# Kernel optimization log

Measured on AMD Instinct MI355X. Metric: run time of the kernel, lower is better.

## Reference

```python
import jax, jax.numpy as jnp
import numpy as np

SCALES = (32.0, 64.0, 128.0, 256.0)
RATIOS = (0.5, 1.0, 2.0)
STRIDE = 16
KEEP = 2000          # pre-NMS top-k
TOPK = 300           # post-NMS top-k
MIN_SIZE = 16.0
SCORE_THRESH = 0.05
NMS_THRESH = 0.7


def static_anchors():
    a = []
    for s in SCALES:
        for r in RATIOS:
            w = s * r ** 0.5
            h = s / r ** 0.5
            a.append((-w / 2, -h / 2, w / 2, h / 2))
    return jnp.asarray(a, jnp.float32)  # [12,4]


def generate_anchors(h, w):
    base = static_anchors()
    sx = jnp.arange(w, dtype=jnp.float32) * STRIDE + STRIDE / 2
    sy = jnp.arange(h, dtype=jnp.float32) * STRIDE + STRIDE / 2
    yy, xx = jnp.meshgrid(sy, sx, indexing='ij')
    xs, ys = xx.reshape(-1), yy.reshape(-1)
    shifts = jnp.stack((xs, ys, xs, ys), axis=1)            # [HW,4]
    return (base[None, :, :] + shifts[:, None, :]).reshape(-1, 4)  # [HW*12,4]


def apply_deltas(anchors, d):
    # bbox reg weights are all 1.0
    aw = anchors[..., 2] - anchors[..., 0]
    ah = anchors[..., 3] - anchors[..., 1]
    ax = anchors[..., 0] + aw * 0.5
    ay = anchors[..., 1] + ah * 0.5
    x = ax + d[..., 0] * aw
    y = ay + d[..., 1] * ah
    w = aw * jnp.exp(d[..., 2])
    h = ah * jnp.exp(d[..., 3])
    return jnp.stack((x - w * 0.5, y - h * 0.5, x + w * 0.5, y + h * 0.5), axis=-1)


def conv2d(x, w, b, pad):
    y = jax.lax.conv_general_dilated(x, w, (1, 1), [(pad, pad), (pad, pad)],
                                     dimension_numbers=('NCHW', 'OIHW', 'NCHW'))
    return y + b[None, :, None, None]


def nms_fixed(boxes, scores, valid):
    # boxes already sorted by descending score; greedy NMS with fixed shapes.
    area = (boxes[:, 2] - boxes[:, 0]) * (boxes[:, 3] - boxes[:, 1])
    lt = jnp.maximum(boxes[:, None, :2], boxes[None, :, :2])
    rb = jnp.minimum(boxes[:, None, 2:], boxes[None, :, 2:])
    wh = jnp.clip(rb - lt, 0.0)
    inter = wh[..., 0] * wh[..., 1]
    iou = inter / jnp.maximum(area[:, None] + area[None, :] - inter, 1e-6)
    n = boxes.shape[0]

    def body(i, state):
        keep, supp = state
        k = jnp.logical_and(~supp[i], True)
        keep = keep.at[i].set(k)
        supp = jnp.logical_or(supp, jnp.logical_and(k, iou[i] > NMS_THRESH))
        return keep, supp

    keep, _ = jax.lax.fori_loop(0, n, body, (jnp.zeros(n, bool), ~valid))
    masked = jnp.where(keep, scores, -jnp.inf)
    top_s, top_i = jax.lax.top_k(masked, TOPK)
    ok = top_s > -jnp.inf
    out_boxes = jnp.where(ok[:, None], boxes[top_i], 0.0)
    out_scores = jnp.where(ok, top_s, 0.0)
    return out_boxes, out_scores


def rpn_forward(fx, w1, b1, w2, b2, w3, b3, img_h, img_w):
    _, _, H, W = fx.shape
    x = jax.nn.relu(conv2d(fx, w1, b1, 1))        # [1,512,H,W]
    ox = conv2d(x, w2, b2, 0)                     # [1,12,H,W]
    ax = conv2d(x, w3, b3, 0)                     # [1,48,H,W]
    anchors = generate_anchors(H, W)              # [A,4]
    ox = jnp.transpose(ox, (0, 2, 3, 1)).reshape(-1)                     # [A]
    ax = jnp.transpose(ax.reshape(1, 12, 4, H, W), (0, 3, 4, 1, 2)).reshape(-1, 4)  # [A,4]
    px = apply_deltas(anchors, ax)                # [A,4]
    s = jax.nn.sigmoid(ox)
    top_s, idx = jax.lax.top_k(s, KEEP)           # pre-NMS filter
    b = px[idx]
    x1 = jnp.clip(b[:, 0], 0.0, img_w)
    x2 = jnp.clip(b[:, 2], 0.0, img_w)
    y1 = jnp.clip(b[:, 1], 0.0, img_h)
    y2 = jnp.clip(b[:, 3], 0.0, img_h)
    boxes = jnp.stack((x1, y1, x2, y2), axis=1)
    valid = ((x2 - x1) >= MIN_SIZE) & ((y2 - y1) >= MIN_SIZE) & (top_s >= SCORE_THRESH)
    out_boxes, out_scores = nms_fixed(boxes, top_s, valid)
    return jnp.concatenate((out_boxes, out_scores[:, None]), axis=1)  # [TOPK,5]


def setup_inputs() -> dict:
    key = jax.random.key(0)
    ks = jax.random.split(key, 4)
    fx = jax.random.normal(ks[0], (1, 1024, 64, 64), jnp.float32)
    w1 = jax.random.normal(ks[1], (512, 1024, 3, 3), jnp.float32) * 0.01
    w2 = jax.random.normal(ks[2], (12, 512, 1, 1), jnp.float32) * 0.01
    w3 = jax.random.normal(ks[3], (48, 512, 1, 1), jnp.float32) * 0.01
    return {"fx": fx, "w1": w1, "b1": jnp.zeros((512,), jnp.float32),
            "w2": w2, "b2": jnp.zeros((12,), jnp.float32),
            "w3": w3, "b3": jnp.zeros((48,), jnp.float32),
            "img_h": 1024, "img_w": 1024}


def reference(fx, w1, b1, w2, b2, w3, b3, img_h, img_w):
    return rpn_forward(fx, w1, b1, w2, b2, w3, b3, float(img_h), float(img_w))
```

## Files before the change

kernel.cpp:

```cpp
#include <hip/hip_runtime.h>
#include <math.h>

typedef unsigned int u32;
typedef unsigned long long u64;
typedef unsigned short u16;

typedef float f32x16 __attribute__((ext_vector_type(16)));
typedef short bf16x8 __attribute__((ext_vector_type(8)));

#define A_TOTAL 49152
#define NKEEP 2000
#define NTOPK 300
#define SORTN 4096

#define OFF_PACC   0u
#define OFF_POX    8388608u
#define OFF_BOXES  16777216u
#define OFF_SCORES 17563648u
#define OFF_HIST   17760256u
#define OFF_KEYS   18022400u
#define OFF_CAND5  18055168u
#define OFF_MASK   18096128u
#define OFF_MISC   18620416u

__global__ __launch_bounds__(256) void k_init(u32* __restrict__ hist, u64* __restrict__ keys,
                                              u32* __restrict__ misc, float* __restrict__ out) {
    int t = blockIdx.x * 256 + threadIdx.x;
    if (t < 65536) hist[t] = 0u;
    if (t < SORTN) keys[t] = 0ull;
    if (t < NTOPK * 5) out[t] = 0.f;
    if (t == 0) misc[0] = 0u;
}

__device__ __forceinline__ u16 f2bf(float v) {
    u32 u = __float_as_uint(v);
    return (u16)((u + 0x7FFFu + ((u >> 16) & 1u)) >> 16);
}
__device__ __forceinline__ float bf2f(u16 h) { return __uint_as_float(((u32)h) << 16); }
__device__ __forceinline__ void split3(float v, u16& h, u16& m, u16& l) {
    h = f2bf(v);
    float r1 = v - bf2f(h);
    m = f2bf(r1);
    float r2 = r1 - bf2f(m);
    l = f2bf(r2);
}
__device__ __forceinline__ bf16x8 ldsfrag(const u16* p) {
    const u64* q = (const u64*)p;
    union { u64 w[2]; bf16x8 v; } x;
    x.w[0] = q[0];
    x.w[1] = q[1];
    return x.v;
}

__global__ __launch_bounds__(512, 4) void k_conv1m(const float* __restrict__ fx, const float* __restrict__ w1,
                                                   float* __restrict__ pacc) {
    __shared__ u16 sA[3 * 9472];
    __shared__ u16 sB[3 * 3600];
    const int tid = threadIdx.x;
    const int lane = tid & 63;
    const int wid = tid >> 6;
    const int cgw = wid >> 2;
    const int pgw = wid & 3;
    const int n = lane & 31;
    const int g = lane >> 5;
    const int bpx = blockIdx.x;
    const int y0 = (bpx >> 2) * 8, x0 = (bpx & 3) * 16;
    const int co0 = blockIdx.y * 64;
    const int kh = blockIdx.z;
    const int ci_base = kh * 512;

    int wg[9], wlA[9];
    u32 wbm = 0u;
#pragma unroll
    for (int j = 0; j < 9; j++) {
        int e = tid + j * 512;
        int co = e / 72, q = e - co * 72;
        int f0 = q * 2;
        int t0 = f0 % 9, c0 = f0 / 9;
        wg[j] = co * 9216 + f0;
        wlA[j] = co * 148 + t0 * 16 + c0;
        if (t0 == 8) wbm |= (1u << j);
    }
    int fg0[6], fl[6];
#pragma unroll
    for (int j = 0; j < 6; j++) {
        int idx = tid + j * 512;
        bool wr = idx < 2880;
        int ci = idx / 180, rem = idx - ci * 180;
        int hy = rem / 18, hx = rem - hy * 18;
        int gy = y0 + hy - 1, gx = x0 + hx - 1;
        bool ok = wr && gy >= 0 && gy < 64 && gx >= 0 && gx < 64;
        fg0[j] = ok ? (ci * 4096 + gy * 64 + gx) : -1;
        fl[j] = wr ? (rem * 20 + ci) : -1;
    }

    f32x16 acc;
    double accD[16];
#pragma unroll
    for (int i = 0; i < 16; i++) { acc[i] = 0.f; accD[i] = 0.0; }

    float pw[18], pf[6];
    {
        const float* wp = w1 + (size_t)co0 * 9216 + (size_t)ci_base * 9;
#pragma unroll
        for (int j = 0; j < 9; j++) { pw[2 * j] = wp[wg[j]]; pw[2 * j + 1] = wp[wg[j] + 1]; }
        const float* fp = fx + (size_t)ci_base * 4096;
#pragma unroll
        for (int j = 0; j < 6; j++) pf[j] = (fg0[j] >= 0) ? fp[fg0[j]] : 0.f;
    }

#pragma unroll 1
    for (int c = 0; c < 32; c++) {
        __syncthreads();
#pragma unroll
        for (int j = 0; j < 9; j++) {
            u16 h, m, l;
            int iA = wlA[j];
            int iB = iA + (((wbm >> j) & 1u) ? -127 : 16);
            split3(pw[2 * j], h, m, l);
            sA[iA] = h; sA[9472 + iA] = m; sA[18944 + iA] = l;
            split3(pw[2 * j + 1], h, m, l);
            sA[iB] = h; sA[9472 + iB] = m; sA[18944 + iB] = l;
        }
#pragma unroll
        for (int j = 0; j < 6; j++) {
            if (fl[j] >= 0) {
                u16 h, m, l;
                split3(pf[j], h, m, l);
                sB[fl[j]] = h; sB[3600 + fl[j]] = m; sB[7200 + fl[j]] = l;
            }
        }
        __syncthreads();
        if (c < 31) {
            const float* wp = w1 + (size_t)co0 * 9216 + (size_t)(ci_base + (c + 1) * 16) * 9;
#pragma unroll
            for (int j = 0; j < 9; j++) { pw[2 * j] = wp[wg[j]]; pw[2 * j + 1] = wp[wg[j] + 1]; }
            const float* fp = fx + (size_t)(ci_base + (c + 1) * 16) * 4096;
#pragma unroll
            for (int j = 0; j < 6; j++) pf[j] = (fg0[j] >= 0) ? fp[fg0[j]] : 0.f;
        }

#pragma unroll 1
        for (int dy = 0; dy < 3; dy++) {
#pragma unroll
            for (int dx = 0; dx < 3; dx++) {
                const int tap = dy * 3 + dx;
                const int aoff = (cgw * 32 + n) * 148 + tap * 16 + g * 8;
                bf16x8 ah = ldsfrag(&sA[aoff]);
                bf16x8 am = ldsfrag(&sA[9472 + aoff]);
                bf16x8 al = ldsfrag(&sA[18944 + aoff]);
                const int loc = (pgw * 2 + (n >> 4) + dy) * 18 + (n & 15) + dx;
                const int boff = loc * 20 + g * 8;
                bf16x8 bh = ldsfrag(&sB[boff]);
                bf16x8 bm = ldsfrag(&sB[3600 + boff]);
                bf16x8 bl = ldsfrag(&sB[7200 + boff]);
                acc = __builtin_amdgcn_mfma_f32_32x32x16_bf16(ah, bh, acc, 0, 0, 0);
                acc = __builtin_amdgcn_mfma_f32_32x32x16_bf16(ah, bm, acc, 0, 0, 0);
                acc = __builtin_amdgcn_mfma_f32_32x32x16_bf16(am, bh, acc, 0, 0, 0);
                acc = __builtin_amdgcn_mfma_f32_32x32x16_bf16(ah, bl, acc, 0, 0, 0);
                acc = __builtin_amdgcn_mfma_f32_32x32x16_bf16(am, bm, acc, 0, 0, 0);
                acc = __builtin_amdgcn_mfma_f32_32x32x16_bf16(al, bh, acc, 0, 0, 0);
            }
#pragma unroll
            for (int i = 0; i < 16; i++) { accD[i] += (double)acc[i]; acc[i] = 0.f; }
        }
    }

    {
        int p = pgw * 32 + n;
        int py = p >> 4, pxx = p & 15;
        int gp = (y0 + py) * 64 + x0 + pxx;
        const int row_hi = 4 * g;
#pragma unroll
        for (int rg = 0; rg < 16; rg++) {
            int co = co0 + cgw * 32 + (rg & 3) + 8 * (rg >> 2) + row_hi;
            pacc[(size_t)kh * 2097152 + (size_t)co * 4096 + gp] = (float)accD[rg];
        }
    }
}

__global__ __launch_bounds__(256) void k_comb(float* __restrict__ x, const float* __restrict__ p1,
                                              const float* __restrict__ b1) {
    int i = blockIdx.x * 256 + threadIdx.x;
    double v = (double)x[i] + (double)p1[i] + (double)b1[i >> 12];
    x[i] = fmaxf((float)v, 0.f);
}

__global__ __launch_bounds__(256) void k_conv23(const float* __restrict__ x,
                                                const float* __restrict__ w2, const float* __restrict__ w3,
                                                double* __restrict__ pox) {
    __shared__ float xs[32 * 64];
    __shared__ float wsh[60 * 128];
    const int tid = threadIdx.x;
    const int px0 = blockIdx.x * 64;
    const int cib = blockIdx.y * 128;
    const int px = tid & 63;
    const int og = tid >> 6;

#pragma unroll
    for (int k = 0; k < 30; k++) {
        int e = tid + k * 256;
        int o = e >> 7, ci = e & 127;
        float wv = (o < 12) ? w2[o * 512 + cib + ci] : w3[(size_t)(o - 12) * 512 + cib + ci];
        wsh[o * 128 + ci] = wv;
    }

    double acc[15];
#pragma unroll
    for (int j = 0; j < 15; j++) acc[j] = 0.0;

#pragma unroll 1
    for (int ch = 0; ch < 4; ch++) {
        __syncthreads();
#pragma unroll
        for (int k = 0; k < 8; k++) {
            int e = tid + k * 256;
            int ci = e >> 6, p = e & 63;
            xs[ci * 64 + p] = x[(size_t)(cib + ch * 32 + ci) * 4096 + px0 + p];
        }
        __syncthreads();
#pragma unroll 1
        for (int ci = 0; ci < 32; ci++) {
            double xd = (double)xs[ci * 64 + px];
            const float* wrow = &wsh[ch * 32 + ci];
#pragma unroll
            for (int j = 0; j < 15; j++)
                acc[j] = fma(xd, (double)wrow[(og * 15 + j) * 128], acc[j]);
        }
    }
#pragma unroll
    for (int j = 0; j < 15; j++) {
        int o = og * 15 + j;
        pox[((size_t)o * 4 + blockIdx.y) * 4096 + px0 + px] = acc[j];
    }
}

__global__ __launch_bounds__(256) void k_boxes(const double* __restrict__ pox,
                                               const float* __restrict__ b2, const float* __restrict__ b3,
                                               const int* __restrict__ imh, const int* __restrict__ imw,
                                               float* __restrict__ boxes, float* __restrict__ scores,
                                               u32* __restrict__ hist) {
    int idx = blockIdx.x * 256 + threadIdx.x;
    if (idx >= A_TOTAL) return;
    int px = idx / 12, a = idx - px * 12;

    double t = 0.0;
#pragma unroll
    for (int q = 0; q < 4; q++) t += pox[((size_t)a * 4 + q) * 4096 + px];
    float o = (float)(t + (double)b2[a]);
    float s = (float)(1.0 / (1.0 + exp(-(double)o)));
    scores[idx] = s;
    atomicAdd(&hist[__float_as_uint(s) >> 16], 1u);

    float d[4];
#pragma unroll
    for (int c = 0; c < 4; c++) {
        int oo = 12 + a * 4 + c;
        double u = 0.0;
#pragma unroll
        for (int q = 0; q < 4; q++) u += pox[((size_t)oo * 4 + q) * 4096 + px];
        d[c] = (float)(u + (double)b3[a * 4 + c]);
    }

    int py = px >> 6, pxx = px & 63;
    double cx = pxx * 16.0 + 8.0, cy = py * 16.0 + 8.0;
    int si = a / 3, ri = a - si * 3;
    double scale = (double)(32 << si);
    double ratio = 0.5 * (double)(1 << ri);
    double sq = sqrt(ratio);
    double aw = scale * sq, ah = scale / sq;
    double xc = cx + (double)d[0] * aw;
    double yc = cy + (double)d[1] * ah;
    double wv = aw * exp((double)d[2]);
    double hv = ah * exp((double)d[3]);
    float W = (float)imw[0], H = (float)imh[0];
    float x1 = fminf(fmaxf((float)(xc - wv * 0.5), 0.f), W);
    float x2 = fminf(fmaxf((float)(xc + wv * 0.5), 0.f), W);
    float y1 = fminf(fmaxf((float)(yc - hv * 0.5), 0.f), H);
    float y2 = fminf(fmaxf((float)(yc + hv * 0.5), 0.f), H);
    boxes[(size_t)idx * 4 + 0] = x1;
    boxes[(size_t)idx * 4 + 1] = y1;
    boxes[(size_t)idx * 4 + 2] = x2;
    boxes[(size_t)idx * 4 + 3] = y2;
}

__global__ __launch_bounds__(256) void k_scanhist(const u32* __restrict__ hist, u32* __restrict__ misc) {
    __shared__ u32 csum[256];
    __shared__ u32 cb[256];
    __shared__ int s_cidx;
    __shared__ u32 s_cacc;
    int t = threadIdx.x;
    u32 sum = 0;
    const uint4* h4 = (const uint4*)(hist + t * 256);
    for (int j = 0; j < 64; j++) { uint4 v = h4[j]; sum += v.x + v.y + v.z + v.w; }
    csum[t] = sum;
    __syncthreads();
    if (t == 0) {
        u32 acc = 0;
        int c = 255;
        for (; c > 0; c--) {
            if (acc + csum[c] >= NKEEP) break;
            acc += csum[c];
        }
        s_cidx = c;
        s_cacc = acc;
    }
    __syncthreads();
    cb[t] = hist[s_cidx * 256 + t];
    __syncthreads();
    if (t == 0) {
        u32 acc = s_cacc;
        int b = 255;
        for (; b > 0; b--) {
            acc += cb[b];
            if (acc >= NKEEP) break;
        }
        misc[1] = (u32)(s_cidx * 256 + b);
    }
}

__global__ __launch_bounds__(256) void k_compact(const float* __restrict__ scores, u32* __restrict__ misc,
                                                 u64* __restrict__ keys) {
    int idx = blockIdx.x * 256 + threadIdx.x;
    if (idx >= A_TOTAL) return;
    u32 bits = __float_as_uint(scores[idx]);
    if ((bits >> 16) >= misc[1]) {
        u32 slot = atomicAdd(&misc[0], 1u);
        if (slot < SORTN) keys[slot] = ((u64)bits << 32) | (u64)(~(u32)idx);
    }
}

__global__ __launch_bounds__(1024) void k_sort(const u64* __restrict__ keys, const float* __restrict__ boxes,
                                               float* __restrict__ cand5, u64* __restrict__ suppws) {
    __shared__ u64 lk[SORTN];
    int t = threadIdx.x;
#pragma unroll
    for (int r = 0; r < 4; r++) lk[r * 1024 + t] = keys[r * 1024 + t];
    for (int kk = 2; kk <= SORTN; kk <<= 1) {
        for (int jj = kk >> 1; jj > 0; jj >>= 1) {
            __syncthreads();
#pragma unroll
            for (int rep = 0; rep < 4; rep++) {
                int i = rep * 1024 + t;
                int ixj = i ^ jj;
                if (ixj > i) {
                    u64 a = lk[i], b = lk[ixj];
                    bool sw = ((i & kk) == 0) ? (a < b) : (a > b);
                    if (sw) { lk[i] = b; lk[ixj] = a; }
                }
            }
        }
    }
    __syncthreads();
#pragma unroll
    for (int rep = 0; rep < 2; rep++) {
        int i = rep * 1024 + t;
        bool suppb = true;
        float c0 = 0.f, c1 = 0.f, c2 = 0.f, c3 = 0.f, cs = 0.f;
        if (i < NKEEP) {
            u64 key = lk[i];
            u32 idx = ~(u32)(key & 0xFFFFFFFFull);
            cs = __uint_as_float((u32)(key >> 32));
            c0 = boxes[(size_t)idx * 4 + 0];
            c1 = boxes[(size_t)idx * 4 + 1];
            c2 = boxes[(size_t)idx * 4 + 2];
            c3 = boxes[(size_t)idx * 4 + 3];
            bool valid = ((c2 - c0) >= 16.f) && ((c3 - c1) >= 16.f) && (cs >= 0.05f);
            suppb = !valid;
        }
        cand5[i * 5 + 0] = c0;
        cand5[i * 5 + 1] = c1;
        cand5[i * 5 + 2] = c2;
        cand5[i * 5 + 3] = c3;
        cand5[i * 5 + 4] = cs;
        u64 bal = __ballot(suppb ? 1 : 0);
        if ((t & 63) == 0) suppws[i >> 6] = bal;
    }
}

__global__ __launch_bounds__(64) void k_mask(const float* __restrict__ cand5, u64* __restrict__ mask) {
    __shared__ float cb[64][5];
    int t = threadIdx.x;
    int bi = blockIdx.y, bj = blockIdx.x;
    int j = bj * 64 + t;
    {
        float b0 = cand5[j * 5 + 0], b1v = cand5[j * 5 + 1], b2v = cand5[j * 5 + 2], b3v = cand5[j * 5 + 3];
        cb[t][0] = b0; cb[t][1] = b1v; cb[t][2] = b2v; cb[t][3] = b3v;
        cb[t][4] = (b2v - b0) * (b3v - b1v);
    }
    __syncthreads();
    int i = bi * 64 + t;
    float r0 = cand5[i * 5 + 0], r1 = cand5[i * 5 + 1], r2 = cand5[i * 5 + 2], r3 = cand5[i * 5 + 3];
    float ra = (r2 - r0) * (r3 - r1);
    u64 bits = 0ull;
#pragma unroll 4
    for (int c = 0; c < 64; c++) {
        float lx = fmaxf(r0, cb[c][0]);
        float ly = fmaxf(r1, cb[c][1]);
        float rx = fminf(r2, cb[c][2]);
        float ry = fminf(r3, cb[c][3]);
        float w = fmaxf(rx - lx, 0.f);
        float h = fmaxf(ry - ly, 0.f);
        float inter = w * h;
        float iou = inter / fmaxf(ra + cb[c][4] - inter, 1e-6f);
        if (iou > 0.7f) bits |= (1ull << c);
    }
    mask[(size_t)i * 32 + bj] = bits;
}

__global__ __launch_bounds__(64) void k_scan(const u64* __restrict__ mask, const float* __restrict__ cand5,
                                             const u64* __restrict__ suppws, float* __restrict__ out) {
    int lane = threadIdx.x;
    u64 supp = (lane < 32) ? suppws[lane] : 0ull;
    u64 bufA[8], bufB[8];
    float dA[8], dB[8];
#pragma unroll
    for (int k = 0; k < 8; k++) {
        bufA[k] = (lane < 32) ? mask[(size_t)k * 32 + lane] : 0ull;
        dA[k] = (lane < 5) ? cand5[k * 5 + lane] : 0.f;
    }
    int kcount = 0;
    for (int gq = 0; gq < 256; gq++) {
        int base = gq * 8;
        if (gq < 255) {
            int nb = base + 8;
#pragma unroll
            for (int k = 0; k < 8; k++) {
                bufB[k] = (lane < 32) ? mask[(size_t)(nb + k) * 32 + lane] : 0ull;
                dB[k] = (lane < 5) ? cand5[(nb + k) * 5 + lane] : 0.f;
            }
        }
        int w = gq >> 3;
        u64 cur = __shfl(supp, w);
#pragma unroll
        for (int k = 0; k < 8; k++) {
            int i = base + k;
            if (i < NKEEP && !((cur >> (i & 63)) & 1ull)) {
                if (kcount < NTOPK) {
                    if (lane < 5) out[kcount * 5 + lane] = dA[k];
                    kcount++;
                }
                supp |= bufA[k];
                cur |= __shfl(bufA[k], w);
            }
        }
        if (kcount >= NTOPK) return;
#pragma unroll
        for (int k = 0; k < 8; k++) { bufA[k] = bufB[k]; dA[k] = dB[k]; }
    }
}

extern "C" void kernel_launch(void* const* d_in, const int* in_sizes, int n_in,
                              void* d_out, int out_size, void* d_ws, size_t ws_size,
                              hipStream_t stream) {
    (void)in_sizes; (void)n_in; (void)out_size; (void)ws_size;
    const float* fx = (const float*)d_in[0];
    const float* w1 = (const float*)d_in[1];
    const float* b1 = (const float*)d_in[2];
    const float* w2 = (const float*)d_in[3];
    const float* b2 = (const float*)d_in[4];
    const float* w3 = (const float*)d_in[5];
    const float* b3 = (const float*)d_in[6];
    const int* imh = (const int*)d_in[7];
    const int* imw = (const int*)d_in[8];

    char* ws = (char*)d_ws;
    float*  pacc   = (float*)(ws + OFF_PACC);
    double* pox    = (double*)(ws + OFF_POX);
    float*  boxes  = (float*)(ws + OFF_BOXES);
    float*  scores = (float*)(ws + OFF_SCORES);
    u32*    hist   = (u32*)(ws + OFF_HIST);
    u64*    keys   = (u64*)(ws + OFF_KEYS);
    float*  cand5  = (float*)(ws + OFF_CAND5);
    u64*    mask   = (u64*)(ws + OFF_MASK);
    u32*    misc   = (u32*)(ws + OFF_MISC);
    u64*    suppws = (u64*)(ws + OFF_MISC + 64);
    float*  out    = (float*)d_out;

    k_init<<<256, 256, 0, stream>>>(hist, keys, misc, out);
    k_conv1m<<<dim3(32, 8, 2), 512, 0, stream>>>(fx, w1, pacc);
    k_comb<<<8192, 256, 0, stream>>>(pacc, pacc + 2097152, b1);
    k_conv23<<<dim3(64, 4), 256, 0, stream>>>(pacc, w2, w3, pox);
    k_boxes<<<192, 256, 0, stream>>>(pox, b2, b3, imh, imw, boxes, scores, hist);
    k_scanhist<<<1, 256, 0, stream>>>(hist, misc);
    k_compact<<<192, 256, 0, stream>>>(scores, misc, keys);
    k_sort<<<1, 1024, 0, stream>>>(keys, boxes, cand5, suppws);
    k_mask<<<dim3(32, 32), 64, 0, stream>>>(cand5, mask);
    k_scan<<<1, 64, 0, stream>>>(mask, cand5, suppws, out);
}
```

Baseline: 560.8 us.

## Rework conv1 staging: paired weight stores, 2-deep fx prefetch, co-major block order

The 3-D grid becomes a 1-D grid ordered so that the eight output-channel blocks for the same pixel tile run next to each other, which is meant to improve L2 reuse of the feature map. Weight staging now pairs two consecutive input channels for the same tap and writes each of the three bf16 split planes with one 32-bit LDS store instead of two 16-bit stores. Feature loads are prefetched two chunks ahead to hide global latency. The launch bound no longer requests four blocks per CU, so the compiler may use more registers at the cost of occupancy, and the extra prefetch buffers add register pressure.

```diff
diff --git a/kernel.cpp b/kernel.cpp
--- a/kernel.cpp
+++ b/kernel.cpp
@@ -52,10 +52,11 @@
     return x.v;
 }
 
-__global__ __launch_bounds__(512, 4) void k_conv1m(const float* __restrict__ fx, const float* __restrict__ w1,
-                                                   float* __restrict__ pacc) {
+__global__ __launch_bounds__(512) void k_conv1m(const float* __restrict__ fx, const float* __restrict__ w1,
+                                                float* __restrict__ pacc) {
     __shared__ u16 sA[3 * 9472];
     __shared__ u16 sB[3 * 3600];
+    u32* const sA32 = (u32*)sA;
     const int tid = threadIdx.x;
     const int lane = tid & 63;
     const int wid = tid >> 6;
@@ -63,23 +64,23 @@
     const int pgw = wid & 3;
     const int n = lane & 31;
     const int g = lane >> 5;
-    const int bpx = blockIdx.x;
+    const int bid = blockIdx.x;
+    const int yb = bid & 7;
+    const int rest = bid >> 3;
+    const int bpx = rest & 31;
+    const int kh = rest >> 5;
     const int y0 = (bpx >> 2) * 8, x0 = (bpx & 3) * 16;
-    const int co0 = blockIdx.y * 64;
-    const int kh = blockIdx.z;
+    const int co0 = yb * 64;
     const int ci_base = kh * 512;
 
-    int wg[9], wlA[9];
-    u32 wbm = 0u;
+    int wgp[9], wlp[9];
 #pragma unroll
     for (int j = 0; j < 9; j++) {
-        int e = tid + j * 512;
-        int co = e / 72, q = e - co * 72;
-        int f0 = q * 2;
-        int t0 = f0 % 9, c0 = f0 / 9;
-        wg[j] = co * 9216 + f0;
-        wlA[j] = co * 148 + t0 * 16 + c0;
-        if (t0 == 8) wbm |= (1u << j);
+        int p = tid + j * 512;
+        int co = p / 72, q = p - co * 72;
+        int a = q & 7, b = q >> 3;
+        wgp[j] = co * 9216 + (2 * a) * 9 + b;
+        wlp[j] = co * 74 + b * 8 + a;
     }
     int fg0[6], fl[6];
 #pragma unroll
@@ -99,14 +100,18 @@
 #pragma unroll
     for (int i = 0; i < 16; i++) { acc[i] = 0.f; accD[i] = 0.0; }
 
-    float pw[18], pf[6];
+    float pw[18], pfA[6], pfB[6];
     {
         const float* wp = w1 + (size_t)co0 * 9216 + (size_t)ci_base * 9;
 #pragma unroll
-        for (int j = 0; j < 9; j++) { pw[2 * j] = wp[wg[j]]; pw[2 * j + 1] = wp[wg[j] + 1]; }
-        const float* fp = fx + (size_t)ci_base * 4096;
-#pragma unroll
-        for (int j = 0; j < 6; j++) pf[j] = (fg0[j] >= 0) ? fp[fg0[j]] : 0.f;
+        for (int j = 0; j < 9; j++) { pw[2 * j] = wp[wgp[j]]; pw[2 * j + 1] = wp[wgp[j] + 9]; }
+        const float* f0 = fx + (size_t)ci_base * 4096;
+        const float* f1 = fx + (size_t)(ci_base + 16) * 4096;
+#pragma unroll
+        for (int j = 0; j < 6; j++) {
+            pfA[j] = (fg0[j] >= 0) ? f0[fg0[j]] : 0.f;
+            pfB[j] = (fg0[j] >= 0) ? f1[fg0[j]] : 0.f;
+        }
     }
 
 #pragma unroll 1
@@ -114,19 +119,18 @@
         __syncthreads();
 #pragma unroll
         for (int j = 0; j < 9; j++) {
-            u16 h, m, l;
-            int iA = wlA[j];
-            int iB = iA + (((wbm >> j) & 1u) ? -127 : 16);
-            split3(pw[2 * j], h, m, l);
-            sA[iA] = h; sA[9472 + iA] = m; sA[18944 + iA] = l;
-            split3(pw[2 * j + 1], h, m, l);
-            sA[iB] = h; sA[9472 + iB] = m; sA[18944 + iB] = l;
+            u16 h0, m0, l0, h1, m1, l1;
+            split3(pw[2 * j], h0, m0, l0);
+            split3(pw[2 * j + 1], h1, m1, l1);
+            sA32[wlp[j]] = (u32)h0 | ((u32)h1 << 16);
+            sA32[4736 + wlp[j]] = (u32)m0 | ((u32)m1 << 16);
+            sA32[9472 + wlp[j]] = (u32)l0 | ((u32)l1 << 16);
         }
 #pragma unroll
         for (int j = 0; j < 6; j++) {
             if (fl[j] >= 0) {
                 u16 h, m, l;
-                split3(pf[j], h, m, l);
+                split3(pfA[j], h, m, l);
                 sB[fl[j]] = h; sB[3600 + fl[j]] = m; sB[7200 + fl[j]] = l;
             }
         }
@@ -134,10 +138,14 @@
         if (c < 31) {
             const float* wp = w1 + (size_t)co0 * 9216 + (size_t)(ci_base + (c + 1) * 16) * 9;
 #pragma unroll
-            for (int j = 0; j < 9; j++) { pw[2 * j] = wp[wg[j]]; pw[2 * j + 1] = wp[wg[j] + 1]; }
-            const float* fp = fx + (size_t)(ci_base + (c + 1) * 16) * 4096;
-#pragma unroll
-            for (int j = 0; j < 6; j++) pf[j] = (fg0[j] >= 0) ? fp[fg0[j]] : 0.f;
+            for (int j = 0; j < 9; j++) { pw[2 * j] = wp[wgp[j]]; pw[2 * j + 1] = wp[wgp[j] + 9]; }
+        }
+#pragma unroll
+        for (int j = 0; j < 6; j++) pfA[j] = pfB[j];
+        if (c < 30) {
+            const float* fp = fx + (size_t)(ci_base + (c + 2) * 16) * 4096;
+#pragma unroll
+            for (int j = 0; j < 6; j++) pfB[j] = (fg0[j] >= 0) ? fp[fg0[j]] : 0.f;
         }
 
 #pragma unroll 1
@@ -478,7 +486,7 @@
     float*  out    = (float*)d_out;
 
     k_init<<<256, 256, 0, stream>>>(hist, keys, misc, out);
-    k_conv1m<<<dim3(32, 8, 2), 512, 0, stream>>>(fx, w1, pacc);
+    k_conv1m<<<512, 512, 0, stream>>>(fx, w1, pacc);
     k_comb<<<8192, 256, 0, stream>>>(pacc, pacc + 2097152, b1);
     k_conv23<<<dim3(64, 4), 256, 0, stream>>>(pacc, w2, w3, pox);
     k_boxes<<<192, 256, 0, stream>>>(pox, b2, b3, imh, imw, boxes, scores, hist);
```

Measured after the change: 554.8 us. Within noise of the previous version (-1.1%).
